# Kernel tuning notes

Measured on AMD Instinct MI355X. Metric: run time of the kernel, lower is better.

The kernel has to match this reference:

```python
import jax, jax.numpy as jnp
import numpy as np

N_SRC, N_DST, DEG = 100000, 50000, 16
NODE_IN, EDGE_IN, HID = 128, 64, 64
E = N_DST * DEG


def sparsemax(z):
    # z: [..., K]; sparsemax along last axis (Martins & Astudillo)
    z = z - jnp.max(z, axis=-1, keepdims=True)
    zs = -jnp.sort(-z, axis=-1)  # descending sort
    k_range = jnp.arange(1, z.shape[-1] + 1, dtype=z.dtype)
    cs = jnp.cumsum(zs, axis=-1)
    is_gt = (1.0 + k_range * zs > cs).astype(z.dtype)
    k = jnp.max(is_gt * k_range, axis=-1, keepdims=True)
    tau = (jnp.sum(is_gt * zs, axis=-1, keepdims=True) - 1.0) / k
    return jnp.maximum(z - tau, 0.0)


def setup_inputs() -> dict:
    key = jax.random.key(0)
    ks = jax.random.split(key, 8)
    s = 0.02
    return {
        "node_features": jax.random.normal(ks[0], (N_SRC, NODE_IN), jnp.float32),
        "edge_features": jax.random.normal(ks[1], (E, EDGE_IN), jnp.float32),
        "src_idx": jax.random.randint(ks[2], (E,), 0, N_SRC, jnp.int32),
        "We": s * jax.random.normal(ks[3], (EDGE_IN, HID), jnp.float32),
        "be": jnp.zeros((HID,), jnp.float32),
        "Wa": s * jax.random.normal(ks[4], (EDGE_IN, HID), jnp.float32),
        "ba": jnp.zeros((HID,), jnp.float32),
        "wa": s * jax.random.normal(ks[5], (HID,), jnp.float32),
        "Wo": s * jax.random.normal(ks[6], (NODE_IN + HID, HID), jnp.float32),
        "bo": jnp.zeros((HID,), jnp.float32),
        "Wn": s * jax.random.normal(ks[7], (NODE_IN + HID, HID), jnp.float32),
        "bn": jnp.zeros((HID,), jnp.float32),
        "n_dst": N_DST,
        "deg": DEG,
    }


def reference(node_features, edge_features, src_idx, We, be, Wa, ba, wa, Wo, bo, Wn, bn, n_dst, deg):
    # dropout is identity in eval / p=0
    h_dst = node_features[:n_dst]                               # [n_dst, node_in]
    # message_func: per-edge transforms
    e_out = jax.nn.relu(edge_features @ We + be)                # [E, hid]
    a = jax.nn.leaky_relu((edge_features @ Wa + ba) @ wa)       # [E]
    h_src_e = node_features[src_idx]                            # gather [E, node_in]
    m = jax.nn.relu(jnp.concatenate([h_src_e, e_out], axis=-1) @ Wo + bo)  # [E, hid]
    # reduce_func: mailbox is [n_dst, deg, .] (fixed in-degree graph)
    a = a.reshape(n_dst, deg)
    m = m.reshape(n_dst, deg, -1)
    alpha = sparsemax(a)                                        # [n_dst, deg]
    h_neigh = jnp.einsum('nd,ndh->nh', alpha, m)                # [n_dst, hid]
    # node update
    return jax.nn.relu(jnp.concatenate([h_dst, h_neigh], axis=-1) @ Wn + bn)
```

## Files before the change

kernel.cpp:

```cpp
#include <hip/hip_runtime.h>


#define ND 50000

typedef __bf16 bf16x8 __attribute__((ext_vector_type(8)));
typedef float f32x4 __attribute__((ext_vector_type(4)));

__device__ __forceinline__ void sync_wave() {
  asm volatile("s_waitcnt lgkmcnt(0)" ::: "memory");
}

__device__ __forceinline__ unsigned short f2bf(float x) {
  unsigned u = __float_as_uint(x);
  u += 0x7fffu + ((u >> 16) & 1u);
  return (unsigned short)(u >> 16);
}

union Frag8 { bf16x8 v; unsigned u32[4]; };

__device__ __forceinline__ bf16x8 pack8(const float* fr) {
  Frag8 f;
  #pragma unroll
  for (int j = 0; j < 4; ++j) {
    unsigned lo = __float_as_uint(fr[2 * j]) + 0x8000u;
    unsigned hi = __float_as_uint(fr[2 * j + 1]) + 0x8000u;
    f.u32[j] = __builtin_amdgcn_perm(hi, lo, 0x07060302);
  }
  return f.v;
}

#define MFMA(a, b, c) __builtin_amdgcn_mfma_f32_16x16x32_bf16((a), (b), (c), 0, 0, 0)

extern "C" __global__ void gteast_prep(const float* __restrict__ Wa,
                                       const float* __restrict__ ba,
                                       const float* __restrict__ wa,
                                       float* __restrict__ vc) {
  __shared__ float red[260];
  const int tid = threadIdx.x, k = tid >> 2, p = tid & 3;
  float s = 0.f;
  for (int h = 16 * p; h < 16 * p + 16; ++h) s += Wa[k * 64 + h] * wa[h];
  red[tid] = s;
  if (tid < 4) {
    float sc = 0.f;
    for (int h = 16 * tid; h < 16 * tid + 16; ++h) sc += ba[h] * wa[h];
    red[256 + tid] = sc;
  }
  __syncthreads();
  if (p == 0) vc[k] = red[4 * k] + red[4 * k + 1] + red[4 * k + 2] + red[4 * k + 3];
  if (tid == 0) vc[64] = red[256] + red[257] + red[258] + red[259];
}

extern "C" __global__ void __launch_bounds__(256, 3)
gteast_edge(const float* __restrict__ nf, const float* __restrict__ ef,
            const int* __restrict__ src_idx,
            const float* __restrict__ We, const float* __restrict__ be,
            const float* __restrict__ Wo, const float* __restrict__ bo,
            const float* __restrict__ vc,
            float* __restrict__ hn_out) {
  __shared__ unsigned short WeT[64 * 72];
  __shared__ unsigned short WoT[64 * 200];
  __shared__ unsigned short Elds[4][16 * 72];
  __shared__ float vls[68];

  const int tid = threadIdx.x;
  for (int i = tid; i < 64 * 64; i += 256) {
    int k = i >> 6, n = i & 63;
    WeT[n * 72 + k] = f2bf(We[i]);
  }
  for (int i = tid; i < 192 * 64; i += 256) {
    int k = i >> 6, n = i & 63;
    WoT[n * 200 + k] = f2bf(Wo[i]);
  }
  if (tid < 65) vls[tid] = vc[tid];
  __syncthreads();

  const int lane = tid & 63, w = tid >> 6;
  const int q = lane >> 4, t = lane & 15;
  const int wid = blockIdx.x * 4 + w;
  if (wid * 8 >= ND) return;

  unsigned short* E = Elds[w];
  const float cval = vls[64];
  float beL[4], boL[4];
  #pragma unroll
  for (int nt = 0; nt < 4; ++nt) { beL[nt] = be[nt * 16 + t]; boL[nt] = bo[nt * 16 + t]; }
  float vsl[16];
  #pragma unroll
  for (int j = 0; j < 8; ++j) { vsl[j] = vls[q * 8 + j]; vsl[8 + j] = vls[32 + q * 8 + j]; }

  const int si0 = src_idx[wid * 128 + lane];
  const int si1 = src_idx[wid * 128 + 64 + lane];

  const long ebase = (long)(wid * 128);

  float4 efn[4];
  {
    const float* er = ef + (ebase + t) * 64 + q * 8;
    efn[0] = *reinterpret_cast<const float4*>(er);
    efn[1] = *reinterpret_cast<const float4*>(er + 4);
    efn[2] = *reinterpret_cast<const float4*>(er + 32);
    efn[3] = *reinterpret_cast<const float4*>(er + 36);
  }
  float hraw[32];
  {
    const int s0 = __shfl(si0, t);
    const float* hp = nf + (long)s0 * 128 + q * 8;
    #pragma unroll
    for (int kc = 0; kc < 4; ++kc) {
      float4 a0 = *reinterpret_cast<const float4*>(hp + kc * 32);
      float4 a1 = *reinterpret_cast<const float4*>(hp + kc * 32 + 4);
      hraw[kc * 8 + 0] = a0.x; hraw[kc * 8 + 1] = a0.y; hraw[kc * 8 + 2] = a0.z; hraw[kc * 8 + 3] = a0.w;
      hraw[kc * 8 + 4] = a1.x; hraw[kc * 8 + 5] = a1.y; hraw[kc * 8 + 6] = a1.z; hraw[kc * 8 + 7] = a1.w;
    }
  }

  for (int it = 0; it < 8; ++it) {
    const int n = wid * 8 + it;
    const int itn = it < 7 ? it + 1 : 7;

    float fe[16];
    fe[0] = efn[0].x; fe[1] = efn[0].y; fe[2] = efn[0].z; fe[3] = efn[0].w;
    fe[4] = efn[1].x; fe[5] = efn[1].y; fe[6] = efn[1].z; fe[7] = efn[1].w;
    fe[8] = efn[2].x; fe[9] = efn[2].y; fe[10] = efn[2].z; fe[11] = efn[2].w;
    fe[12] = efn[3].x; fe[13] = efn[3].y; fe[14] = efn[3].z; fe[15] = efn[3].w;
    {
      const float* er = ef + (ebase + itn * 16 + t) * 64 + q * 8;
      efn[0] = *reinterpret_cast<const float4*>(er);
      efn[1] = *reinterpret_cast<const float4*>(er + 4);
      efn[2] = *reinterpret_cast<const float4*>(er + 32);
      efn[3] = *reinterpret_cast<const float4*>(er + 36);
    }

    float ap = 0.f;
    #pragma unroll
    for (int j = 0; j < 16; ++j) ap += fe[j] * vsl[j];
    ap += __shfl_xor(ap, 16);
    ap += __shfl_xor(ap, 32);
    float a = ap + cval;
    a = a > 0.f ? a : 0.01f * a;

    const bf16x8 e0 = pack8(fe), e1 = pack8(fe + 8);
    #pragma unroll
    for (int nt = 0; nt < 4; ++nt) {
      f32x4 c = {0.f, 0.f, 0.f, 0.f};
      c = MFMA(e0, *reinterpret_cast<const bf16x8*>(&WeT[(nt * 16 + t) * 72 + q * 8]), c);
      c = MFMA(e1, *reinterpret_cast<const bf16x8*>(&WeT[(nt * 16 + t) * 72 + 32 + q * 8]), c);
      #pragma unroll
      for (int r = 0; r < 4; ++r) {
        float vv = fmaxf(c[r] + beL[nt], 0.f);
        E[(4 * q + r) * 72 + nt * 16 + t] = f2bf(vv);
      }
    }
    sync_wave();

    bf16x8 af[6];
    #pragma unroll
    for (int kc = 0; kc < 4; ++kc) af[kc] = pack8(hraw + kc * 8);
    af[4] = *reinterpret_cast<const bf16x8*>(&E[t * 72 + q * 8]);
    af[5] = *reinterpret_cast<const bf16x8*>(&E[t * 72 + 32 + q * 8]);

    {
      const int sn = (itn < 4) ? __shfl(si0, 16 * itn + t)
                               : __shfl(si1, 16 * (itn - 4) + t);
      const float* hp = nf + (long)sn * 128 + q * 8;
      #pragma unroll
      for (int kc = 0; kc < 4; ++kc) {
        float4 a0 = *reinterpret_cast<const float4*>(hp + kc * 32);
        float4 a1 = *reinterpret_cast<const float4*>(hp + kc * 32 + 4);
        hraw[kc * 8 + 0] = a0.x; hraw[kc * 8 + 1] = a0.y; hraw[kc * 8 + 2] = a0.z; hraw[kc * 8 + 3] = a0.w;
        hraw[kc * 8 + 4] = a1.x; hraw[kc * 8 + 5] = a1.y; hraw[kc * 8 + 6] = a1.z; hraw[kc * 8 + 7] = a1.w;
      }
    }

    f32x4 accM[4];
    #pragma unroll
    for (int nt = 0; nt < 4; ++nt) {
      f32x4 c = {0.f, 0.f, 0.f, 0.f};
      #pragma unroll
      for (int kc = 0; kc < 6; ++kc)
        c = MFMA(af[kc], *reinterpret_cast<const bf16x8*>(&WoT[(nt * 16 + t) * 200 + kc * 32 + q * 8]), c);
      #pragma unroll
      for (int r = 0; r < 4; ++r) c[r] = fmaxf(c[r] + boL[nt], 0.f);
      accM[nt] = c;
    }
    sync_wave();

    float z = a;
    #pragma unroll
    for (int k = 2; k <= 16; k <<= 1) {
      #pragma unroll
      for (int j = k >> 1; j > 0; j >>= 1) {
        float o = __shfl_xor(z, j);
        const bool upper = (t & j) != 0;
        const bool desc = (t & k) == 0;
        z = (upper != desc) ? fmaxf(z, o) : fminf(z, o);
      }
    }
    float cs = z;
    #pragma unroll
    for (int off = 1; off < 16; off <<= 1) {
      float o = __shfl_up(cs, off, 16);
      cs += (t >= off) ? o : 0.f;
    }
    const bool gt = 1.f + (float)(t + 1) * z > cs;
    float kf = gt ? (float)(t + 1) : 0.f;
    float sv = gt ? z : 0.f;
    #pragma unroll
    for (int m = 1; m < 16; m <<= 1) {
      kf = fmaxf(kf, __shfl_xor(kf, m));
      sv += __shfl_xor(sv, m);
    }
    const float tau = (sv - 1.f) / kf;
    const float alpha = fmaxf(a - tau, 0.f);

    float al[4];
    #pragma unroll
    for (int r = 0; r < 4; ++r) al[r] = __shfl(alpha, 4 * q + r);
    float p[4];
    #pragma unroll
    for (int nt = 0; nt < 4; ++nt) {
      p[nt] = al[0] * accM[nt][0] + al[1] * accM[nt][1] +
              al[2] * accM[nt][2] + al[3] * accM[nt][3];
      p[nt] += __shfl_xor(p[nt], 16);
      p[nt] += __shfl_xor(p[nt], 32);
    }
    const float pown = (q == 0) ? p[0] : (q == 1) ? p[1] : (q == 2) ? p[2] : p[3];
    hn_out[(long)n * 64 + lane] = pown;
  }
}

extern "C" __global__ void __launch_bounds__(256, 3)
gteast_out(const float* __restrict__ nf, const float* __restrict__ Wn,
           const float* __restrict__ bn, float* __restrict__ out) {
  __shared__ unsigned short WnT[64 * 200];
  const int tid = threadIdx.x;
  for (int i = tid; i < 192 * 64; i += 256) {
    int k = i >> 6, nn = i & 63;
    WnT[nn * 200 + k] = f2bf(Wn[i]);
  }
  __syncthreads();

  const int lane = tid & 63, w = tid >> 6, q = lane >> 4, t = lane & 15;
  const int tile = blockIdx.x * 4 + w;
  if (tile >= ND / 16) return;
  const int r0 = tile * 16;

  float bnL[4];
  #pragma unroll
  for (int nt = 0; nt < 4; ++nt) bnL[nt] = bn[nt * 16 + t];

  float raw[8];
  bf16x8 af[6];
  const float* hp = nf + (long)(r0 + t) * 128 + q * 8;
  #pragma unroll
  for (int kc = 0; kc < 4; ++kc) {
    float4 a0 = *reinterpret_cast<const float4*>(hp + kc * 32);
    float4 a1 = *reinterpret_cast<const float4*>(hp + kc * 32 + 4);
    raw[0] = a0.x; raw[1] = a0.y; raw[2] = a0.z; raw[3] = a0.w;
    raw[4] = a1.x; raw[5] = a1.y; raw[6] = a1.z; raw[7] = a1.w;
    af[kc] = pack8(raw);
  }
  const float* gp = out + (long)(r0 + t) * 64 + q * 8;
  #pragma unroll
  for (int kc = 0; kc < 2; ++kc) {
    float4 a0 = *reinterpret_cast<const float4*>(gp + kc * 32);
    float4 a1 = *reinterpret_cast<const float4*>(gp + kc * 32 + 4);
    raw[0] = a0.x; raw[1] = a0.y; raw[2] = a0.z; raw[3] = a0.w;
    raw[4] = a1.x; raw[5] = a1.y; raw[6] = a1.z; raw[7] = a1.w;
    af[4 + kc] = pack8(raw);
  }

  #pragma unroll
  for (int nt = 0; nt < 4; ++nt) {
    f32x4 c = {0.f, 0.f, 0.f, 0.f};
    #pragma unroll
    for (int kc = 0; kc < 6; ++kc)
      c = MFMA(af[kc], *reinterpret_cast<const bf16x8*>(&WnT[(nt * 16 + t) * 200 + kc * 32 + q * 8]), c);
    #pragma unroll
    for (int r = 0; r < 4; ++r)
      out[(long)(r0 + 4 * q + r) * 64 + nt * 16 + t] = fmaxf(c[r] + bnL[nt], 0.f);
  }
}

extern "C" void kernel_launch(void* const* d_in, const int* in_sizes, int n_in,
                              void* d_out, int out_size, void* d_ws, size_t ws_size,
                              hipStream_t stream) {
  const float* nf = (const float*)d_in[0];
  const float* ef = (const float*)d_in[1];
  const int* si   = (const int*)d_in[2];
  const float* We = (const float*)d_in[3];
  const float* be = (const float*)d_in[4];
  const float* Wa = (const float*)d_in[5];
  const float* ba = (const float*)d_in[6];
  const float* wa = (const float*)d_in[7];
  const float* Wo = (const float*)d_in[8];
  const float* bo = (const float*)d_in[9];
  const float* Wn = (const float*)d_in[10];
  const float* bn = (const float*)d_in[11];
  float* out = (float*)d_out;
  float* vc = (float*)d_ws;

  gteast_prep<<<1, 256, 0, stream>>>(Wa, ba, wa, vc);
  gteast_edge<<<1563, 256, 0, stream>>>(nf, ef, si, We, be, Wo, bo, vc, out);
  gteast_out<<<782, 256, 0, stream>>>(nf, Wn, bn, out);
}
```

Baseline: 386.7 us.

## Keep edge-transform output in registers via transposed MFMA and permuted Wo rows

Swaps the MFMA operand order in the edge transform so each lane holds a transposed tile of e_out, packing it directly into the A fragments of the second GEMM instead of round-tripping through per-wave LDS. To make that register layout match, the e_out rows of Wo are permuted when staged into shared memory, and the bias is loaded per-q as float4. This removes the LDS scratch buffer and both wave-level waits, and the launch bound is raised to 4 blocks per SM, which may force register spills.

```diff
diff --git a/kernel.cpp b/kernel.cpp
--- a/kernel.cpp
+++ b/kernel.cpp
@@ -5,10 +5,6 @@
 
 typedef __bf16 bf16x8 __attribute__((ext_vector_type(8)));
 typedef float f32x4 __attribute__((ext_vector_type(4)));
-
-__device__ __forceinline__ void sync_wave() {
-  asm volatile("s_waitcnt lgkmcnt(0)" ::: "memory");
-}
 
 __device__ __forceinline__ unsigned short f2bf(float x) {
   unsigned u = __float_as_uint(x);
@@ -50,7 +46,7 @@
   if (tid == 0) vc[64] = red[256] + red[257] + red[258] + red[259];
 }
 
-extern "C" __global__ void __launch_bounds__(256, 3)
+extern "C" __global__ void __launch_bounds__(256, 4)
 gteast_edge(const float* __restrict__ nf, const float* __restrict__ ef,
             const int* __restrict__ src_idx,
             const float* __restrict__ We, const float* __restrict__ be,
@@ -59,7 +55,6 @@
             float* __restrict__ hn_out) {
   __shared__ unsigned short WeT[64 * 72];
   __shared__ unsigned short WoT[64 * 200];
-  __shared__ unsigned short Elds[4][16 * 72];
   __shared__ float vls[68];
 
   const int tid = threadIdx.x;
@@ -69,7 +64,12 @@
   }
   for (int i = tid; i < 192 * 64; i += 256) {
     int k = i >> 6, n = i & 63;
-    WoT[n * 200 + k] = f2bf(Wo[i]);
+    int kk = k;
+    if (k >= 128) {
+      int h = k - 128;
+      kk = 128 + (h & 32) + ((h >> 2) & 3) * 8 + ((h >> 4) & 1) * 4 + (h & 3);
+    }
+    WoT[n * 200 + kk] = f2bf(Wo[i]);
   }
   if (tid < 65) vls[tid] = vc[tid];
   __syncthreads();
@@ -79,11 +79,14 @@
   const int wid = blockIdx.x * 4 + w;
   if (wid * 8 >= ND) return;
 
-  unsigned short* E = Elds[w];
   const float cval = vls[64];
-  float beL[4], boL[4];
-  #pragma unroll
-  for (int nt = 0; nt < 4; ++nt) { beL[nt] = be[nt * 16 + t]; boL[nt] = bo[nt * 16 + t]; }
+  float boL[4];
+  float4 beQ[4];
+  #pragma unroll
+  for (int nt = 0; nt < 4; ++nt) {
+    boL[nt] = bo[nt * 16 + t];
+    beQ[nt] = *reinterpret_cast<const float4*>(be + nt * 16 + 4 * q);
+  }
   float vsl[16];
   #pragma unroll
   for (int j = 0; j < 8; ++j) { vsl[j] = vls[q * 8 + j]; vsl[8 + j] = vls[32 + q * 8 + j]; }
@@ -140,24 +143,24 @@
     a = a > 0.f ? a : 0.01f * a;
 
     const bf16x8 e0 = pack8(fe), e1 = pack8(fe + 8);
-    #pragma unroll
-    for (int nt = 0; nt < 4; ++nt) {
-      f32x4 c = {0.f, 0.f, 0.f, 0.f};
-      c = MFMA(e0, *reinterpret_cast<const bf16x8*>(&WeT[(nt * 16 + t) * 72 + q * 8]), c);
-      c = MFMA(e1, *reinterpret_cast<const bf16x8*>(&WeT[(nt * 16 + t) * 72 + 32 + q * 8]), c);
-      #pragma unroll
-      for (int r = 0; r < 4; ++r) {
-        float vv = fmaxf(c[r] + beL[nt], 0.f);
-        E[(4 * q + r) * 72 + nt * 16 + t] = f2bf(vv);
+    bf16x8 af[6];
+    {
+      float eo[16];
+      #pragma unroll
+      for (int nt = 0; nt < 4; ++nt) {
+        f32x4 c = {0.f, 0.f, 0.f, 0.f};
+        c = MFMA(*reinterpret_cast<const bf16x8*>(&WeT[(nt * 16 + t) * 72 + q * 8]), e0, c);
+        c = MFMA(*reinterpret_cast<const bf16x8*>(&WeT[(nt * 16 + t) * 72 + 32 + q * 8]), e1, c);
+        #pragma unroll
+        for (int r = 0; r < 4; ++r)
+          eo[nt * 4 + r] = fmaxf(c[r] + beQ[nt][r], 0.f);
       }
-    }
-    sync_wave();
-
-    bf16x8 af[6];
+      af[4] = pack8(eo);
+      af[5] = pack8(eo + 8);
+    }
+
     #pragma unroll
     for (int kc = 0; kc < 4; ++kc) af[kc] = pack8(hraw + kc * 8);
-    af[4] = *reinterpret_cast<const bf16x8*>(&E[t * 72 + q * 8]);
-    af[5] = *reinterpret_cast<const bf16x8*>(&E[t * 72 + 32 + q * 8]);
 
     {
       const int sn = (itn < 4) ? __shfl(si0, 16 * itn + t)
@@ -183,7 +186,6 @@
       for (int r = 0; r < 4; ++r) c[r] = fmaxf(c[r] + boL[nt], 0.f);
       accM[nt] = c;
     }
-    sync_wave();
 
     float z = a;
     #pragma unroll
```

Result: slower. 656.0 us (+69.6%).

## Precompute per-source-node Wo projection and gather projected rows instead of raw features

Applied to the files above, without the earlier changes.

Splits the message matmul so the node-feature part (nf @ Wo[:128]) is computed once per source node into a bf16 workspace table. The edge kernel then gathers 64-wide bf16 projected rows instead of 128-wide fp32 features, which cuts gather bytes and per-edge MFMA work. The sparsemax bitonic sort is replaced by a rank-count formulation. This adds an extra kernel launch plus a workspace write and read, and adds bf16 rounding of the projected sum. A fallback to the old kernel runs when the workspace is too small.

```diff
diff --git a/kernel.cpp b/kernel.cpp
--- a/kernel.cpp
+++ b/kernel.cpp
@@ -2,6 +2,7 @@
 
 
 #define ND 50000
+#define NS 100000
 
 typedef __bf16 bf16x8 __attribute__((ext_vector_type(8)));
 typedef float f32x4 __attribute__((ext_vector_type(4)));
@@ -14,6 +15,9 @@
   unsigned u = __float_as_uint(x);
   u += 0x7fffu + ((u >> 16) & 1u);
   return (unsigned short)(u >> 16);
+}
+__device__ __forceinline__ float bf2f(unsigned short u) {
+  return __uint_as_float((unsigned)u << 16);
 }
 
 union Frag8 { bf16x8 v; unsigned u32[4]; };
@@ -51,14 +55,52 @@
 }
 
 extern "C" __global__ void __launch_bounds__(256, 3)
-gteast_edge(const float* __restrict__ nf, const float* __restrict__ ef,
-            const int* __restrict__ src_idx,
+gteast_src(const float* __restrict__ nf, const float* __restrict__ Wo,
+           unsigned short* __restrict__ y) {
+  __shared__ unsigned short WuT[64 * 136];
+  const int tid = threadIdx.x;
+  for (int i = tid; i < 128 * 64; i += 256) {
+    int k = i >> 6, n = i & 63;
+    WuT[n * 136 + k] = f2bf(Wo[i]);
+  }
+  __syncthreads();
+
+  const int lane = tid & 63, w = tid >> 6, q = lane >> 4, t = lane & 15;
+  const int tile = blockIdx.x * 4 + w;
+  if (tile >= NS / 16) return;
+  const int r0 = tile * 16;
+
+  float raw[8];
+  bf16x8 af[4];
+  const float* hp = nf + (long)(r0 + t) * 128 + q * 8;
+  #pragma unroll
+  for (int kc = 0; kc < 4; ++kc) {
+    float4 a0 = *reinterpret_cast<const float4*>(hp + kc * 32);
+    float4 a1 = *reinterpret_cast<const float4*>(hp + kc * 32 + 4);
+    raw[0] = a0.x; raw[1] = a0.y; raw[2] = a0.z; raw[3] = a0.w;
+    raw[4] = a1.x; raw[5] = a1.y; raw[6] = a1.z; raw[7] = a1.w;
+    af[kc] = pack8(raw);
+  }
+  #pragma unroll
+  for (int nt = 0; nt < 4; ++nt) {
+    f32x4 c = {0.f, 0.f, 0.f, 0.f};
+    #pragma unroll
+    for (int kc = 0; kc < 4; ++kc)
+      c = MFMA(af[kc], *reinterpret_cast<const bf16x8*>(&WuT[(nt * 16 + t) * 136 + kc * 32 + q * 8]), c);
+    #pragma unroll
+    for (int r = 0; r < 4; ++r)
+      y[(long)(r0 + 4 * q + r) * 64 + nt * 16 + t] = f2bf(c[r]);
+  }
+}
+
+extern "C" __global__ void __launch_bounds__(256, 3)
+gteast_edge(const float* __restrict__ ef, const int* __restrict__ src_idx,
             const float* __restrict__ We, const float* __restrict__ be,
             const float* __restrict__ Wo, const float* __restrict__ bo,
-            const float* __restrict__ vc,
+            const float* __restrict__ vc, const unsigned short* __restrict__ y,
             float* __restrict__ hn_out) {
   __shared__ unsigned short WeT[64 * 72];
-  __shared__ unsigned short WoT[64 * 200];
+  __shared__ unsigned short WoLoT[64 * 72];
   __shared__ unsigned short Elds[4][16 * 72];
   __shared__ float vls[68];
 
@@ -67,9 +109,9 @@
     int k = i >> 6, n = i & 63;
     WeT[n * 72 + k] = f2bf(We[i]);
   }
-  for (int i = tid; i < 192 * 64; i += 256) {
+  for (int i = tid; i < 64 * 64; i += 256) {
     int k = i >> 6, n = i & 63;
-    WoT[n * 200 + k] = f2bf(Wo[i]);
+    WoLoT[n * 72 + k] = f2bf(Wo[(128 + k) * 64 + n]);
   }
   if (tid < 65) vls[tid] = vc[tid];
   __syncthreads();
@@ -101,17 +143,13 @@
     efn[2] = *reinterpret_cast<const float4*>(er + 32);
     efn[3] = *reinterpret_cast<const float4*>(er + 36);
   }
-  float hraw[32];
-  {
-    const int s0 = __shfl(si0, t);
-    const float* hp = nf + (long)s0 * 128 + q * 8;
-    #pragma unroll
-    for (int kc = 0; kc < 4; ++kc) {
-      float4 a0 = *reinterpret_cast<const float4*>(hp + kc * 32);
-      float4 a1 = *reinterpret_cast<const float4*>(hp + kc * 32 + 4);
-      hraw[kc * 8 + 0] = a0.x; hraw[kc * 8 + 1] = a0.y; hraw[kc * 8 + 2] = a0.z; hraw[kc * 8 + 3] = a0.w;
-      hraw[kc * 8 + 4] = a1.x; hraw[kc * 8 + 5] = a1.y; hraw[kc * 8 + 6] = a1.z; hraw[kc * 8 + 7] = a1.w;
-    }
+  unsigned short yv[16];
+  #pragma unroll
+  for (int r = 0; r < 4; ++r) {
+    const int s0 = __shfl(si0, 4 * q + r);
+    const unsigned short* yp = y + (long)s0 * 64 + t;
+    #pragma unroll
+    for (int nt = 0; nt < 4; ++nt) yv[r * 4 + nt] = yp[nt * 16];
   }
 
   for (int it = 0; it < 8; ++it) {
@@ -153,6 +191,171 @@
     }
     sync_wave();
 
+    bf16x8 af4 = *reinterpret_cast<const bf16x8*>(&E[t * 72 + q * 8]);
+    bf16x8 af5 = *reinterpret_cast<const bf16x8*>(&E[t * 72 + 32 + q * 8]);
+
+    f32x4 accM[4];
+    #pragma unroll
+    for (int nt = 0; nt < 4; ++nt) {
+      f32x4 c = {0.f, 0.f, 0.f, 0.f};
+      c = MFMA(af4, *reinterpret_cast<const bf16x8*>(&WoLoT[(nt * 16 + t) * 72 + q * 8]), c);
+      c = MFMA(af5, *reinterpret_cast<const bf16x8*>(&WoLoT[(nt * 16 + t) * 72 + 32 + q * 8]), c);
+      #pragma unroll
+      for (int r = 0; r < 4; ++r)
+        c[r] = fmaxf(c[r] + bf2f(yv[r * 4 + nt]) + boL[nt], 0.f);
+      accM[nt] = c;
+    }
+    sync_wave();
+
+    #pragma unroll
+    for (int r = 0; r < 4; ++r) {
+      const int idx = 16 * itn + 4 * q + r;
+      const int sn = (itn < 4) ? __shfl(si0, idx) : __shfl(si1, idx - 64);
+      const unsigned short* yp = y + (long)sn * 64 + t;
+      #pragma unroll
+      for (int nt = 0; nt < 4; ++nt) yv[r * 4 + nt] = yp[nt * 16];
+    }
+
+    const float z = a;
+    float cp = 0.f, sp = 0.f;
+    #pragma unroll
+    for (int r = 0; r < 4; ++r) {
+      float zj = __shfl(z, 4 * q + r, 16);
+      const bool ge = (zj >= z);
+      cp += ge ? 1.f : 0.f;
+      sp += ge ? zj : 0.f;
+    }
+    cp += __shfl_xor(cp, 16); sp += __shfl_xor(sp, 16);
+    cp += __shfl_xor(cp, 32); sp += __shfl_xor(sp, 32);
+    const bool valid = 1.f + cp * z > sp;
+    float kf = valid ? cp : 0.f;
+    float sv = valid ? sp : 0.f;
+    #pragma unroll
+    for (int m = 1; m < 16; m <<= 1) {
+      float ok = __shfl_xor(kf, m), os = __shfl_xor(sv, m);
+      if (ok > kf) { kf = ok; sv = os; }
+    }
+    const float tau = (sv - 1.f) / kf;
+    const float alpha = fmaxf(a - tau, 0.f);
+
+    float al[4];
+    #pragma unroll
+    for (int r = 0; r < 4; ++r) al[r] = __shfl(alpha, 4 * q + r);
+    float p[4];
+    #pragma unroll
+    for (int nt = 0; nt < 4; ++nt) {
+      p[nt] = al[0] * accM[nt][0] + al[1] * accM[nt][1] +
+              al[2] * accM[nt][2] + al[3] * accM[nt][3];
+      p[nt] += __shfl_xor(p[nt], 16);
+      p[nt] += __shfl_xor(p[nt], 32);
+    }
+    const float pown = (q == 0) ? p[0] : (q == 1) ? p[1] : (q == 2) ? p[2] : p[3];
+    hn_out[(long)n * 64 + lane] = pown;
+  }
+}
+
+extern "C" __global__ void __launch_bounds__(256, 3)
+gteast_edge_fb(const float* __restrict__ nf, const float* __restrict__ ef,
+               const int* __restrict__ src_idx,
+               const float* __restrict__ We, const float* __restrict__ be,
+               const float* __restrict__ Wo, const float* __restrict__ bo,
+               const float* __restrict__ vc,
+               float* __restrict__ hn_out) {
+  __shared__ unsigned short WeT[64 * 72];
+  __shared__ unsigned short WoT[64 * 200];
+  __shared__ unsigned short Elds[4][16 * 72];
+  __shared__ float vls[68];
+
+  const int tid = threadIdx.x;
+  for (int i = tid; i < 64 * 64; i += 256) {
+    int k = i >> 6, n = i & 63;
+    WeT[n * 72 + k] = f2bf(We[i]);
+  }
+  for (int i = tid; i < 192 * 64; i += 256) {
+    int k = i >> 6, n = i & 63;
+    WoT[n * 200 + k] = f2bf(Wo[i]);
+  }
+  if (tid < 65) vls[tid] = vc[tid];
+  __syncthreads();
+
+  const int lane = tid & 63, w = tid >> 6;
+  const int q = lane >> 4, t = lane & 15;
+  const int wid = blockIdx.x * 4 + w;
+  if (wid * 8 >= ND) return;
+
+  unsigned short* E = Elds[w];
+  const float cval = vls[64];
+  float beL[4], boL[4];
+  #pragma unroll
+  for (int nt = 0; nt < 4; ++nt) { beL[nt] = be[nt * 16 + t]; boL[nt] = bo[nt * 16 + t]; }
+  float vsl[16];
+  #pragma unroll
+  for (int j = 0; j < 8; ++j) { vsl[j] = vls[q * 8 + j]; vsl[8 + j] = vls[32 + q * 8 + j]; }
+
+  const int si0 = src_idx[wid * 128 + lane];
+  const int si1 = src_idx[wid * 128 + 64 + lane];
+  const long ebase = (long)(wid * 128);
+
+  float4 efn[4];
+  {
+    const float* er = ef + (ebase + t) * 64 + q * 8;
+    efn[0] = *reinterpret_cast<const float4*>(er);
+    efn[1] = *reinterpret_cast<const float4*>(er + 4);
+    efn[2] = *reinterpret_cast<const float4*>(er + 32);
+    efn[3] = *reinterpret_cast<const float4*>(er + 36);
+  }
+  float hraw[32];
+  {
+    const int s0 = __shfl(si0, t);
+    const float* hp = nf + (long)s0 * 128 + q * 8;
+    #pragma unroll
+    for (int kc = 0; kc < 4; ++kc) {
+      float4 a0 = *reinterpret_cast<const float4*>(hp + kc * 32);
+      float4 a1 = *reinterpret_cast<const float4*>(hp + kc * 32 + 4);
+      hraw[kc * 8 + 0] = a0.x; hraw[kc * 8 + 1] = a0.y; hraw[kc * 8 + 2] = a0.z; hraw[kc * 8 + 3] = a0.w;
+      hraw[kc * 8 + 4] = a1.x; hraw[kc * 8 + 5] = a1.y; hraw[kc * 8 + 6] = a1.z; hraw[kc * 8 + 7] = a1.w;
+    }
+  }
+
+  for (int it = 0; it < 8; ++it) {
+    const int n = wid * 8 + it;
+    const int itn = it < 7 ? it + 1 : 7;
+
+    float fe[16];
+    fe[0] = efn[0].x; fe[1] = efn[0].y; fe[2] = efn[0].z; fe[3] = efn[0].w;
+    fe[4] = efn[1].x; fe[5] = efn[1].y; fe[6] = efn[1].z; fe[7] = efn[1].w;
+    fe[8] = efn[2].x; fe[9] = efn[2].y; fe[10] = efn[2].z; fe[11] = efn[2].w;
+    fe[12] = efn[3].x; fe[13] = efn[3].y; fe[14] = efn[3].z; fe[15] = efn[3].w;
+    {
+      const float* er = ef + (ebase + itn * 16 + t) * 64 + q * 8;
+      efn[0] = *reinterpret_cast<const float4*>(er);
+      efn[1] = *reinterpret_cast<const float4*>(er + 4);
+      efn[2] = *reinterpret_cast<const float4*>(er + 32);
+      efn[3] = *reinterpret_cast<const float4*>(er + 36);
+    }
+
+    float ap = 0.f;
+    #pragma unroll
+    for (int j = 0; j < 16; ++j) ap += fe[j] * vsl[j];
+    ap += __shfl_xor(ap, 16);
+    ap += __shfl_xor(ap, 32);
+    float a = ap + cval;
+    a = a > 0.f ? a : 0.01f * a;
+
+    const bf16x8 e0 = pack8(fe), e1 = pack8(fe + 8);
+    #pragma unroll
+    for (int nt = 0; nt < 4; ++nt) {
+      f32x4 c = {0.f, 0.f, 0.f, 0.f};
+      c = MFMA(e0, *reinterpret_cast<const bf16x8*>(&WeT[(nt * 16 + t) * 72 + q * 8]), c);
+      c = MFMA(e1, *reinterpret_cast<const bf16x8*>(&WeT[(nt * 16 + t) * 72 + 32 + q * 8]), c);
+      #pragma unroll
+      for (int r = 0; r < 4; ++r) {
+        float vv = fmaxf(c[r] + beL[nt], 0.f);
+        E[(4 * q + r) * 72 + nt * 16 + t] = f2bf(vv);
+      }
+    }
+    sync_wave();
+
     bf16x8 af[6];
     #pragma unroll
     for (int kc = 0; kc < 4; ++kc) af[kc] = pack8(hraw + kc * 8);
@@ -185,26 +388,26 @@
     }
     sync_wave();
 
-    float z = a;
+    float zz = a;
     #pragma unroll
     for (int k = 2; k <= 16; k <<= 1) {
       #pragma unroll
       for (int j = k >> 1; j > 0; j >>= 1) {
-        float o = __shfl_xor(z, j);
+        float o = __shfl_xor(zz, j);
         const bool upper = (t & j) != 0;
         const bool desc = (t & k) == 0;
-        z = (upper != desc) ? fmaxf(z, o) : fminf(z, o);
+        zz = (upper != desc) ? fmaxf(zz, o) : fminf(zz, o);
       }
     }
-    float cs = z;
+    float cs = zz;
     #pragma unroll
     for (int off = 1; off < 16; off <<= 1) {
       float o = __shfl_up(cs, off, 16);
       cs += (t >= off) ? o : 0.f;
     }
-    const bool gt = 1.f + (float)(t + 1) * z > cs;
+    const bool gt = 1.f + (float)(t + 1) * zz > cs;
     float kf = gt ? (float)(t + 1) : 0.f;
-    float sv = gt ? z : 0.f;
+    float sv = gt ? zz : 0.f;
     #pragma unroll
     for (int m = 1; m < 16; m <<= 1) {
       kf = fmaxf(kf, __shfl_xor(kf, m));
@@ -300,7 +503,15 @@
   float* out = (float*)d_out;
   float* vc = (float*)d_ws;
 
+  const size_t yneed = 512 + (size_t)NS * 64 * sizeof(unsigned short);
+
   gteast_prep<<<1, 256, 0, stream>>>(Wa, ba, wa, vc);
-  gteast_edge<<<1563, 256, 0, stream>>>(nf, ef, si, We, be, Wo, bo, vc, out);
+  if (ws_size >= yneed) {
+    unsigned short* y = (unsigned short*)((char*)d_ws + 512);
+    gteast_src<<<1563, 256, 0, stream>>>(nf, Wo, y);
+    gteast_edge<<<1563, 256, 0, stream>>>(ef, si, We, be, Wo, bo, vc, y, out);
+  } else {
+    gteast_edge_fb<<<1563, 256, 0, stream>>>(nf, ef, si, We, be, Wo, bo, vc, out);
+  }
   gteast_out<<<782, 256, 0, stream>>>(nf, Wn, bn, out);
 }
```

Result: faster. 373.5 us (-3.4%).
